# Performance work log

Measured on AMD Instinct MI355X. Metric: run time of the kernel, lower is better.

The kernel has to match this reference:

```python
import jax, jax.numpy as jnp
import numpy as np

NUM_HEADS = 4
NUM_GROUPS = 8
EPS = 1e-5


def group_norm(x, gamma, beta):
    B, C, H, W = x.shape
    xg = x.reshape(B, NUM_GROUPS, C // NUM_GROUPS, H, W)
    mean = xg.mean(axis=(2, 3, 4), keepdims=True)
    var = xg.var(axis=(2, 3, 4), keepdims=True)
    xn = ((xg - mean) * jax.lax.rsqrt(var + EPS)).reshape(B, C, H, W)
    return xn * gamma[None, :, None, None] + beta[None, :, None, None]


def setup_inputs() -> dict:
    key = jax.random.key(0)
    k1, k2, k3 = jax.random.split(key, 3)
    B, C, H, W = 16, 512, 32, 32
    x = jax.random.normal(k1, (B, C, H, W), dtype=jnp.float32)
    gn_gamma = jnp.ones((C,), dtype=jnp.float32)
    gn_beta = jnp.zeros((C,), dtype=jnp.float32)
    w_qkv = jax.random.normal(k2, (3 * C, C), dtype=jnp.float32) * 0.02
    w_proj = jax.random.normal(k3, (C, C), dtype=jnp.float32) * 0.02
    b_proj = jnp.zeros((C,), dtype=jnp.float32)
    return {"x": x, "gn_gamma": gn_gamma, "gn_beta": gn_beta,
            "w_qkv": w_qkv, "w_proj": w_proj, "b_proj": b_proj}


def reference(x, gn_gamma, gn_beta, w_qkv, w_proj, b_proj):
    B, C, H, W = x.shape
    nh = NUM_HEADS
    hd = C // nh
    N = H * W

    x_norm = group_norm(x, gn_gamma, gn_beta)
    # 1x1 conv == channel matmul: (B,C,H,W) x (3C,C) -> (B,3C,H,W)
    qkv = jnp.einsum('bchw,dc->bdhw', x_norm, w_qkv)
    qkv = qkv.reshape(B, 3, nh, hd, N)
    q, k, v = qkv[:, 0], qkv[:, 1], qkv[:, 2]  # each (B, nh, hd, N)

    scale = hd ** (-0.5)
    attn = jnp.einsum('bhci,bhcj->bhij', q, k) * scale  # (B, nh, N, N)
    attn = jax.nn.softmax(attn, axis=-1)
    out = jnp.einsum('bhij,bhcj->bhci', attn, v)  # (B, nh, hd, N)
    out = out.reshape(B, C, H, W)

    proj = jnp.einsum('bchw,dc->bdhw', out, w_proj) + b_proj[None, :, None, None]
    return x + proj
```

## Files before the change

### kernel.cpp

```cpp
#include <hip/hip_runtime.h>
#include <stdint.h>

typedef unsigned short u16;
typedef unsigned int u32;
typedef __attribute__((ext_vector_type(8))) short short8;
typedef __attribute__((ext_vector_type(4))) float f32x4;
typedef __attribute__((ext_vector_type(16))) float f32x16;

#define BATCH 16
#define CCH   512
#define NPIX  1024
#define NGRP  8
#define CPG   64
#define NHEAD 4
#define HDIM  128
#define KVBLK 64

__device__ __forceinline__ u16 f2bf(float f) {
  union { float f; u32 u; } v; v.f = f;
  u32 u = v.u;
  u32 r = (u + 0x7FFFu + ((u >> 16) & 1u)) >> 16;
  return (u16)r;
}

__device__ __forceinline__ void gload16(const void* g, void* l) {
  typedef __attribute__((address_space(3))) u32 L;
  typedef __attribute__((address_space(1))) const u32 G;
  __builtin_amdgcn_global_load_lds((G*)(uintptr_t)g, (L*)(u32)(uintptr_t)l, 16, 0, 0);
}

#define CVTPK(dst, a, b) asm("v_cvt_pk_bf16_f32 %0, %1, %2" : "=v"(dst) : "v"(a), "v"(b))
#define PLSWAP(a, b) asm("v_permlane32_swap_b32 %0, %1" : "+v"(a), "+v"(b))

__device__ __forceinline__ short8 rd512(const char* base, int r, int ck, int hi) {
  int byte = ((r >> 2) * 512) +
             ((((r & 3) * 128) + ck * 32 + hi * 16) ^ (((r >> 2) & 15) << 4));
  return *reinterpret_cast<const short8*>(base + byte);
}

__global__ void gn_stats_k(const float* __restrict__ x, float* __restrict__ part) {
  int bg = blockIdx.x >> 3, sl = blockIdx.x & 7;
  const float* p = x + (size_t)bg * (CPG * NPIX) + sl * 8192;
  float s = 0.f, ss = 0.f;
  for (int i = threadIdx.x; i < 2048; i += 256) {
    float4 v = reinterpret_cast<const float4*>(p)[i];
    s  += v.x + v.y + v.z + v.w;
    ss += v.x*v.x + v.y*v.y + v.z*v.z + v.w*v.w;
  }
  for (int o = 32; o > 0; o >>= 1) { s += __shfl_down(s, o); ss += __shfl_down(ss, o); }
  __shared__ float sh[8];
  int wid = threadIdx.x >> 6;
  if ((threadIdx.x & 63) == 0) { sh[wid*2] = s; sh[wid*2+1] = ss; }
  __syncthreads();
  if (threadIdx.x == 0) {
    part[blockIdx.x*2]   = sh[0]+sh[2]+sh[4]+sh[6];
    part[blockIdx.x*2+1] = sh[1]+sh[3]+sh[5]+sh[7];
  }
}

__global__ __launch_bounds__(256) void gn_apply_t(const float* __restrict__ x,
                                                  const float* __restrict__ gamma,
                                                  const float* __restrict__ beta,
                                                  const float* __restrict__ part,
                                                  u16* __restrict__ xnT) {
  const int p0 = blockIdx.x * 64;
  const int c0 = blockIdx.y * 64;
  const int b  = blockIdx.z;
  __shared__ float lt[64][66];

  const int bg = b * NGRP + (c0 >> 6);
  float s = 0.f, ss = 0.f;
  #pragma unroll
  for (int k2 = 0; k2 < 8; ++k2) { s += part[(bg*8 + k2)*2]; ss += part[(bg*8 + k2)*2 + 1]; }
  const float invn = 1.f / (float)(CPG * NPIX);
  const float mean = s * invn;
  const float rstd = rsqrtf(ss * invn - mean * mean + 1e-5f);

  const int t = threadIdx.x;
  #pragma unroll
  for (int pass = 0; pass < 4; ++pass) {
    int c   = c0 + (t >> 4) + pass * 16;
    int pix = p0 + (t & 15) * 4;
    float ga = gamma[c] * rstd;
    float be = beta[c] - mean * ga;
    float4 v = *reinterpret_cast<const float4*>(&x[((size_t)(b*CCH + c)) * NPIX + pix]);
    int pl = (t & 15) * 4, cl = (t >> 4) + pass * 16;
    lt[pl+0][cl] = v.x*ga + be;
    lt[pl+1][cl] = v.y*ga + be;
    lt[pl+2][cl] = v.z*ga + be;
    lt[pl+3][cl] = v.w*ga + be;
  }
  __syncthreads();
  const int pl = t >> 2, cq = (t & 3) * 16;
  u32 wbuf[8];
  #pragma unroll
  for (int e = 0; e < 8; ++e) {
    u16 lo = f2bf(lt[pl][cq + e*2]);
    u16 hi = f2bf(lt[pl][cq + e*2 + 1]);
    wbuf[e] = (u32)lo | ((u32)hi << 16);
  }
  u32* dst = (u32*)&xnT[((size_t)(b*NPIX + p0 + pl)) * CCH + c0 + cq];
  #pragma unroll
  for (int e = 0; e < 8; ++e) dst[e] = wbuf[e];
}

__global__ void f2bf_all(const float* __restrict__ wqkv, const float* __restrict__ wproj,
                         u16* __restrict__ wq, u16* __restrict__ wp, float qs) {
  int i = blockIdx.x * 256 + threadIdx.x;
  float4 v; u16* dst; float sc = 1.f;
  if (i < 196608) {
    v = reinterpret_cast<const float4*>(wqkv)[i];
    if (i < 65536) sc = qs;
    dst = wq + (size_t)i * 4;
  } else {
    v = reinterpret_cast<const float4*>(wproj)[i - 196608];
    dst = wp + (size_t)(i - 196608) * 4;
  }
  u32 lo = (u32)f2bf(v.x*sc) | ((u32)f2bf(v.y*sc) << 16);
  u32 hi = (u32)f2bf(v.z*sc) | ((u32)f2bf(v.w*sc) << 16);
  *reinterpret_cast<uint2*>(dst) = make_uint2(lo, hi);
}

__global__ __launch_bounds__(256, 3) void gemm_qkv(const u16* __restrict__ xnT,
                                                   const u16* __restrict__ wq_bf,
                                                   u16* __restrict__ outQ,
                                                   u16* __restrict__ outK,
                                                   u16* __restrict__ outV) {
  __shared__ __align__(16) char smem[34816];

  const int id = blockIdx.x;
  const int wg = (id & 7) * 192 + (id >> 3);
  const bool mode0 = (wg < 1024);
  int rt, ct;
  if (mode0) { rt = wg >> 3; ct = wg & 7; }
  else       { int w1 = wg - 1024; rt = w1 & 3; ct = w1 >> 2; }

  const char* Ab = mode0 ? (const char*)xnT + (size_t)rt * 131072
                         : (const char*)wq_bf + (size_t)(8 + rt) * 131072;
  const char* Bb = mode0 ? (const char*)wq_bf + (size_t)ct * 131072
                         : (const char*)xnT + (size_t)ct * 131072;

  const int t = threadIdx.x;
  const int lane = t & 63, w = t >> 6;
  const int q = lane & 31, hi = lane >> 5;
  const int rh = (w >> 1) * 64, ch = (w & 1) * 64;

  int soff[4];
  #pragma unroll
  for (int i = 0; i < 4; ++i) {
    int p = w*4096 + i*1024 + lane*16;
    int lrow = p >> 9, off = p & 511;
    int loff = off ^ ((lrow & 15) << 4);
    soff[i] = (lrow*4 + (loff >> 7)) * 1024 + (loff & 127);
  }

  f32x16 a00 = {}, a01 = {}, a10 = {}, a11 = {};

  for (int kt = 0; kt < 8; ++kt) {
    __syncthreads();
    #pragma unroll
    for (int i = 0; i < 4; ++i) {
      gload16(Ab + kt*128 + soff[i], smem + w*4096 + i*1024);
      gload16(Bb + kt*128 + soff[i], smem + 16384 + w*4096 + i*1024);
    }
    __syncthreads();
    #pragma unroll
    for (int ck = 0; ck < 4; ++ck) {
      short8 af0 = rd512(smem,         rh + q,      ck, hi);
      short8 af1 = rd512(smem,         rh + 32 + q, ck, hi);
      short8 bf0 = rd512(smem + 16384, ch + q,      ck, hi);
      short8 bf1 = rd512(smem + 16384, ch + 32 + q, ck, hi);
      a00 = __builtin_amdgcn_mfma_f32_32x32x16_bf16(af0, bf0, a00, 0, 0, 0);
      a01 = __builtin_amdgcn_mfma_f32_32x32x16_bf16(af0, bf1, a01, 0, 0, 0);
      a10 = __builtin_amdgcn_mfma_f32_32x32x16_bf16(af1, bf0, a10, 0, 0, 0);
      a11 = __builtin_amdgcn_mfma_f32_32x32x16_bf16(af1, bf1, a11, 0, 0, 0);
    }
  }

  __syncthreads();
  u16* Dt = (u16*)smem;
  #pragma unroll
  for (int r = 0; r < 16; ++r) {
    int ar = (r & 3) + 8*(r >> 2) + 4*hi;
    Dt[(rh +      ar) * 136 + ch +      q] = f2bf(a00[r]);
    Dt[(rh +      ar) * 136 + ch + 32 + q] = f2bf(a01[r]);
    Dt[(rh + 32 + ar) * 136 + ch +      q] = f2bf(a10[r]);
    Dt[(rh + 32 + ar) * 136 + ch + 32 + q] = f2bf(a11[r]);
  }
  __syncthreads();

  const int rl = t >> 1, hoff = (t & 1) * 64;
  uint4 buf[8];
  const uint4* s4 = reinterpret_cast<const uint4*>(&Dt[rl*136 + hoff]);
  #pragma unroll
  for (int e = 0; e < 8; ++e) buf[e] = s4[e];

  u16* gdst;
  if (mode0) {
    const int tok0 = rt * 128;
    const int b = tok0 >> 10, pix0 = tok0 & 1023;
    const int h = ct & 3;
    u16* base = (ct >= 4) ? outK : outQ;
    gdst = base + ((size_t)((b*NHEAD + h)) * NPIX + pix0 + rl) * HDIM + hoff;
  } else {
    const int m0 = rt * 128, tok0 = ct * 128;
    const int b = tok0 >> 10, pix0 = tok0 & 1023;
    gdst = outV + ((size_t)(b*CCH + m0 + rl)) * NPIX + pix0 + hoff;
  }
  uint4* g4 = reinterpret_cast<uint4*>(gdst);
  #pragma unroll
  for (int e = 0; e < 8; ++e) g4[e] = buf[e];
}

__global__ __launch_bounds__(256, 3) void gemm_proj(const u16* __restrict__ wp_bf,
                                                    const u16* __restrict__ attnO,
                                                    const float* __restrict__ xres,
                                                    const float* __restrict__ bias,
                                                    float* __restrict__ outF) {
  __shared__ __align__(16) char smem[32768];

  const int id = blockIdx.x;
  const int wg = (id & 7) * 64 + (id >> 3);
  const int rt = wg & 3, ct = wg >> 2;

  const char* Ab = (const char*)wp_bf + (size_t)rt * 131072;
  const char* Bb = (const char*)attnO + (size_t)ct * 131072;

  const int t = threadIdx.x;
  const int lane = t & 63, w = t >> 6;
  const int q = lane & 31, hi = lane >> 5;
  const int rh = (w >> 1) * 64, ch = (w & 1) * 64;

  int soff[4];
  #pragma unroll
  for (int i = 0; i < 4; ++i) {
    int p = w*4096 + i*1024 + lane*16;
    int lrow = p >> 9, off = p & 511;
    int loff = off ^ ((lrow & 15) << 4);
    soff[i] = (lrow*4 + (loff >> 7)) * 1024 + (loff & 127);
  }

  f32x16 a00 = {}, a01 = {}, a10 = {}, a11 = {};

  for (int kt = 0; kt < 8; ++kt) {
    __syncthreads();
    #pragma unroll
    for (int i = 0; i < 4; ++i) {
      gload16(Ab + kt*128 + soff[i], smem + w*4096 + i*1024);
      gload16(Bb + kt*128 + soff[i], smem + 16384 + w*4096 + i*1024);
    }
    __syncthreads();
    #pragma unroll
    for (int ck = 0; ck < 4; ++ck) {
      short8 af0 = rd512(smem,         rh + q,      ck, hi);
      short8 af1 = rd512(smem,         rh + 32 + q, ck, hi);
      short8 bf0 = rd512(smem + 16384, ch + q,      ck, hi);
      short8 bf1 = rd512(smem + 16384, ch + 32 + q, ck, hi);
      a00 = __builtin_amdgcn_mfma_f32_32x32x16_bf16(af0, bf0, a00, 0, 0, 0);
      a01 = __builtin_amdgcn_mfma_f32_32x32x16_bf16(af0, bf1, a01, 0, 0, 0);
      a10 = __builtin_amdgcn_mfma_f32_32x32x16_bf16(af1, bf0, a10, 0, 0, 0);
      a11 = __builtin_amdgcn_mfma_f32_32x32x16_bf16(af1, bf1, a11, 0, 0, 0);
    }
  }

  const int m0 = rt * 128, tok0 = ct * 128;
  const int b = tok0 >> 10, pix0 = tok0 & 1023;
  #pragma unroll
  for (int r = 0; r < 16; ++r) {
    int ar = (r & 3) + 8*(r >> 2) + 4*hi;
    int m0r = m0 + rh + ar, m1r = m0 + rh + 32 + ar;
    size_t o00 = ((size_t)(b*CCH + m0r)) * NPIX + pix0 + ch + q;
    size_t o01 = o00 + 32;
    size_t o10 = ((size_t)(b*CCH + m1r)) * NPIX + pix0 + ch + q;
    size_t o11 = o10 + 32;
    outF[o00] = xres[o00] + a00[r] + bias[m0r];
    outF[o01] = xres[o01] + a01[r] + bias[m0r];
    outF[o10] = xres[o10] + a10[r] + bias[m1r];
    outF[o11] = xres[o11] + a11[r] + bias[m1r];
  }
}

__global__ __launch_bounds__(256, 2) void attn_k(const u16* __restrict__ Qt,
                                                 const u16* __restrict__ Kt,
                                                 const u16* __restrict__ Vb,
                                                 u16* __restrict__ attnO) {
  int id = blockIdx.x;
  int swz = (id & 7) * 64 + (id >> 3);
  const int qt = swz & 7;
  const int h  = (swz >> 3) & 3;
  const int b  = swz >> 5;
  const int bh = b * NHEAD + h;

  __shared__ __align__(16) char smem[65536];

  const int t = threadIdx.x;
  const int lane = t & 63, w = t >> 6;
  const int q = lane & 31, hi = lane >> 5;

  const u16*  Qb    = Qt + ((size_t)bh * NPIX + qt*128 + w*32 + q) * HDIM;
  const char* Kbase = (const char*)(Kt + (size_t)bh * NPIX * HDIM);
  const char* Vbase = (const char*)(Vb + ((size_t)b*CCH + h*HDIM) * NPIX);

  short8 qf[8];
  #pragma unroll
  for (int ck = 0; ck < 8; ++ck)
    qf[ck] = *reinterpret_cast<const short8*>(&Qb[ck*16 + hi*8]);

  int koff[4], voff[4];
  #pragma unroll
  for (int i = 0; i < 4; ++i) {
    int d = w*4096 + i*1024 + lane*16;
    int r = d >> 8, cb = d & 255;
    int col = cb ^ ((r & 15) << 4);
    koff[i] = r*256 + col;
    int half = col >> 7, kvb = col & 127;
    voff[i] = (2*r + half)*2048 + kvb;
  }

  const int ksw = (q & 15) << 4;
  const int vsw = (q >> 1) << 4;

  f32x16 of0 = {}, of1 = {}, of2 = {}, of3 = {};
  float l_run = 0.f;
  short8 pf0, pf1, pf2, pf3;

  #pragma unroll
  for (int i = 0; i < 4; ++i) {
    gload16(Kbase + koff[i],            smem +         w*4096 + i*1024);
    gload16(Vbase + voff[i],            smem + 32768 + w*4096 + i*1024);
    gload16(Kbase + (size_t)64*256 + koff[i], smem + 16384 + w*4096 + i*1024);
  }
  asm volatile("s_waitcnt vmcnt(0)" ::: "memory");
  __syncthreads();

  f32x16 s0 = {}, s1 = {};
  #pragma unroll
  for (int ck = 0; ck < 8; ++ck) {
    const short8 kf0 = *reinterpret_cast<const short8*>(smem + q*256      + ((ck*32 + hi*16) ^ ksw));
    const short8 kf1 = *reinterpret_cast<const short8*>(smem + (32+q)*256 + ((ck*32 + hi*16) ^ ksw));
    s0 = __builtin_amdgcn_mfma_f32_32x32x16_bf16(kf0, qf[ck], s0, 0, 0, 0);
    s1 = __builtin_amdgcn_mfma_f32_32x32x16_bf16(kf1, qf[ck], s1, 0, 0, 0);
  }
  {
    float psum = 0.f;
    u32 wg[8], xg[8];
    #pragma unroll
    for (int u = 0; u < 8; ++u) {
      float pa = exp2f(s0[2*u]);  float pb = exp2f(s0[2*u+1]);
      float pc = exp2f(s1[2*u]);  float pd = exp2f(s1[2*u+1]);
      psum += (pa + pb) + (pc + pd);
      CVTPK(wg[u], pa, pb);
      CVTPK(xg[u], pc, pd);
    }
    psum += __shfl_xor(psum, 32);
    l_run += psum;
    PLSWAP(wg[0], wg[2]); PLSWAP(wg[1], wg[3]);
    PLSWAP(wg[4], wg[6]); PLSWAP(wg[5], wg[7]);
    PLSWAP(xg[0], xg[2]); PLSWAP(xg[1], xg[3]);
    PLSWAP(xg[4], xg[6]); PLSWAP(xg[5], xg[7]);
    union { u32 u[4]; short8 s; } a0, a1, a2, a3;
    #pragma unroll
    for (int u = 0; u < 4; ++u) { a0.u[u]=wg[u]; a1.u[u]=wg[4+u]; a2.u[u]=xg[u]; a3.u[u]=xg[4+u]; }
    pf0 = a0.s; pf1 = a1.s; pf2 = a2.s; pf3 = a3.s;
  }

  for (int tt = 0; tt < 16; ++tt) {
    asm volatile("s_waitcnt vmcnt(0)" ::: "memory");
    __syncthreads();

    char* kcur = smem + (((tt+1) & 1) << 14);
    char* vcur = smem + 32768 + ((tt & 1) << 14);

    if (tt + 1 < 16) {
      char* vdst = smem + 32768 + (((tt+1) & 1) << 14);
      #pragma unroll
      for (int i = 0; i < 4; ++i)
        gload16(Vbase + (size_t)(tt+1)*128 + voff[i], vdst + w*4096 + i*1024);
    }
    if (tt + 2 < 16) {
      char* kdst = smem + ((tt & 1) << 14);
      #pragma unroll
      for (int i = 0; i < 4; ++i)
        gload16(Kbase + (size_t)(tt+2)*64*256 + koff[i], kdst + w*4096 + i*1024);
    }

    __builtin_amdgcn_s_setprio(1);
    if (tt + 1 < 16) {
      s0 = {}; s1 = {};
      #pragma unroll
      for (int ck = 0; ck < 8; ++ck) {
        const short8 kf0 = *reinterpret_cast<const short8*>(kcur + q*256      + ((ck*32 + hi*16) ^ ksw));
        const short8 kf1 = *reinterpret_cast<const short8*>(kcur + (32+q)*256 + ((ck*32 + hi*16) ^ ksw));
        s0 = __builtin_amdgcn_mfma_f32_32x32x16_bf16(kf0, qf[ck], s0, 0, 0, 0);
        s1 = __builtin_amdgcn_mfma_f32_32x32x16_bf16(kf1, qf[ck], s1, 0, 0, 0);
      }
    }
    #pragma unroll
    for (int cg = 0; cg < 4; ++cg) {
      const char* vrow = vcur + (cg*16 + (q >> 1))*256;
      const int hb = (q & 1) << 7;
      f32x16 o = (cg == 0) ? of0 : (cg == 1) ? of1 : (cg == 2) ? of2 : of3;
      o = __builtin_amdgcn_mfma_f32_32x32x16_bf16(*reinterpret_cast<const short8*>(vrow + ((hb +  0 + hi*16) ^ vsw)), pf0, o, 0, 0, 0);
      o = __builtin_amdgcn_mfma_f32_32x32x16_bf16(*reinterpret_cast<const short8*>(vrow + ((hb + 32 + hi*16) ^ vsw)), pf1, o, 0, 0, 0);
      o = __builtin_amdgcn_mfma_f32_32x32x16_bf16(*reinterpret_cast<const short8*>(vrow + ((hb + 64 + hi*16) ^ vsw)), pf2, o, 0, 0, 0);
      o = __builtin_amdgcn_mfma_f32_32x32x16_bf16(*reinterpret_cast<const short8*>(vrow + ((hb + 96 + hi*16) ^ vsw)), pf3, o, 0, 0, 0);
      if (cg == 0) of0 = o; else if (cg == 1) of1 = o; else if (cg == 2) of2 = o; else of3 = o;
    }
    __builtin_amdgcn_s_setprio(0);

    if (tt + 1 < 16) {
      float psum = 0.f;
      u32 wg[8], xg[8];
      #pragma unroll
      for (int u = 0; u < 8; ++u) {
        float pa = exp2f(s0[2*u]);  float pb = exp2f(s0[2*u+1]);
        float pc = exp2f(s1[2*u]);  float pd = exp2f(s1[2*u+1]);
        psum += (pa + pb) + (pc + pd);
        CVTPK(wg[u], pa, pb);
        CVTPK(xg[u], pc, pd);
      }
      psum += __shfl_xor(psum, 32);
      l_run += psum;
      PLSWAP(wg[0], wg[2]); PLSWAP(wg[1], wg[3]);
      PLSWAP(wg[4], wg[6]); PLSWAP(wg[5], wg[7]);
      PLSWAP(xg[0], xg[2]); PLSWAP(xg[1], xg[3]);
      PLSWAP(xg[4], xg[6]); PLSWAP(xg[5], xg[7]);
      union { u32 u[4]; short8 s; } a0, a1, a2, a3;
      #pragma unroll
      for (int u = 0; u < 4; ++u) { a0.u[u]=wg[u]; a1.u[u]=wg[4+u]; a2.u[u]=xg[u]; a3.u[u]=xg[4+u]; }
      pf0 = a0.s; pf1 = a1.s; pf2 = a2.s; pf3 = a3.s;
    }
  }

  float inv = 1.f / l_run;
  u16* orow = attnO + ((size_t)(b*NPIX + qt*128 + w*32 + q)) * CCH + h*HDIM;
  #pragma unroll
  for (int cg = 0; cg < 4; ++cg) {
    const f32x16& o = (cg == 0) ? of0 : (cg == 1) ? of1 : (cg == 2) ? of2 : of3;
    #pragma unroll
    for (int u = 0; u < 8; ++u) {
      int c = cg*32 + ((2*u) & 3) + 8*(u >> 1) + 4*hi;
      u32 pk = (u32)f2bf(o[2*u] * inv) | ((u32)f2bf(o[2*u+1] * inv) << 16);
      *reinterpret_cast<u32*>(&orow[c]) = pk;
    }
  }
}

extern "C" void kernel_launch(void* const* d_in, const int* in_sizes, int n_in,
                              void* d_out, int out_size, void* d_ws, size_t ws_size,
                              hipStream_t stream) {
  const float* x     = (const float*)d_in[0];
  const float* gamma = (const float*)d_in[1];
  const float* beta  = (const float*)d_in[2];
  const float* wqkv  = (const float*)d_in[3];
  const float* wproj = (const float*)d_in[4];
  const float* bproj = (const float*)d_in[5];
  float* out = (float*)d_out;

  char* ws = (char*)d_ws;
  float* part   = (float*)ws;
  u16*   xnT    = (u16*)(ws + 8192);
  u16*   wq_bf  = (u16*)(ws + 8192 + (16u<<20));
  u16*   wp_bf  = (u16*)((char*)wq_bf + 1572864);
  u16*   Qt     = (u16*)((char*)wp_bf + 524288);
  u16*   Kt     = (u16*)((char*)Qt + (16u<<20));
  u16*   Vb     = (u16*)((char*)Kt + (16u<<20));
  u16*   attnO  = (u16*)((char*)Vb + (16u<<20));

  const float qs = 0.08838834764831845f * 1.44269504088896f;

  gn_stats_k<<<dim3(1024), dim3(256), 0, stream>>>(x, part);
  gn_apply_t<<<dim3(16, 8, BATCH), dim3(256), 0, stream>>>(x, gamma, beta, part, xnT);
  f2bf_all<<<dim3(1024), dim3(256), 0, stream>>>(wqkv, wproj, wq_bf, wp_bf, qs);

  gemm_qkv<<<dim3(1536), dim3(256), 0, stream>>>(xnT, wq_bf, Qt, Kt, Vb);

  attn_k<<<dim3(512), dim3(256), 0, stream>>>(Qt, Kt, Vb, attnO);

  gemm_proj<<<dim3(512), dim3(256), 0, stream>>>(wp_bf, attnO, x, bproj, out);
}
```

Baseline: 124.7 us.

## Double-buffer LDS tiles in QKV and projection GEMMs with async prefetch

The QKV and projection GEMM kernels now keep two LDS tile buffers (64KB total) so the next K-slice is fetched by global_load_lds while MFMAs run on the current one. This replaces the load-then-sync pattern that stalled on each tile. MFMA sections get raised wave priority. Occupancy hints drop from 3 to 2 blocks per CU because of the larger LDS footprint. The attention kernel's softmax/pack code is factored into a helper, with the row sum split across four partial accumulators.

```diff
diff --git a/kernel.cpp b/kernel.cpp
--- a/kernel.cpp
+++ b/kernel.cpp
@@ -6,6 +6,7 @@
 typedef __attribute__((ext_vector_type(8))) short short8;
 typedef __attribute__((ext_vector_type(4))) float f32x4;
 typedef __attribute__((ext_vector_type(16))) float f32x16;
+typedef __attribute__((ext_vector_type(4))) u32 u32x4;
 
 #define BATCH 16
 #define CCH   512
@@ -36,6 +37,31 @@
   int byte = ((r >> 2) * 512) +
              ((((r & 3) * 128) + ck * 32 + hi * 16) ^ (((r >> 2) & 15) << 4));
   return *reinterpret_cast<const short8*>(base + byte);
+}
+
+__device__ __forceinline__ float softmax_pack(const f32x16& s0, const f32x16& s1, short8* pf) {
+  float ps[4] = {0.f, 0.f, 0.f, 0.f};
+  u32 pw[16];
+  #pragma unroll
+  for (int u = 0; u < 8; ++u) {
+    float pa = exp2f(s0[2*u]);  float pb = exp2f(s0[2*u+1]);
+    float pc = exp2f(s1[2*u]);  float pd = exp2f(s1[2*u+1]);
+    ps[u & 3] += (pa + pb) + (pc + pd);
+    CVTPK(pw[u],     pa, pb);
+    CVTPK(pw[8 + u], pc, pd);
+  }
+  PLSWAP(pw[0], pw[2]);  PLSWAP(pw[1], pw[3]);
+  PLSWAP(pw[4], pw[6]);  PLSWAP(pw[5], pw[7]);
+  PLSWAP(pw[8], pw[10]); PLSWAP(pw[9], pw[11]);
+  PLSWAP(pw[12], pw[14]); PLSWAP(pw[13], pw[15]);
+  #pragma unroll
+  for (int f = 0; f < 4; ++f) {
+    u32x4 t = {pw[f*4], pw[f*4+1], pw[f*4+2], pw[f*4+3]};
+    pf[f] = __builtin_bit_cast(short8, t);
+  }
+  float psum = (ps[0] + ps[1]) + (ps[2] + ps[3]);
+  psum += __shfl_xor(psum, 32);
+  return psum;
 }
 
 __global__ void gn_stats_k(const float* __restrict__ x, float* __restrict__ part) {
@@ -121,12 +147,12 @@
   *reinterpret_cast<uint2*>(dst) = make_uint2(lo, hi);
 }
 
-__global__ __launch_bounds__(256, 3) void gemm_qkv(const u16* __restrict__ xnT,
+__global__ __launch_bounds__(256, 2) void gemm_qkv(const u16* __restrict__ xnT,
                                                    const u16* __restrict__ wq_bf,
                                                    u16* __restrict__ outQ,
                                                    u16* __restrict__ outK,
                                                    u16* __restrict__ outV) {
-  __shared__ __align__(16) char smem[34816];
+  __shared__ __align__(16) char smem[65536];
 
   const int id = blockIdx.x;
   const int wg = (id & 7) * 192 + (id >> 3);
@@ -154,27 +180,39 @@
     soff[i] = (lrow*4 + (loff >> 7)) * 1024 + (loff & 127);
   }
 
-  f32x16 a00 = {}, a01 = {}, a10 = {}, a11 = {};
+  #pragma unroll
+  for (int i = 0; i < 4; ++i) {
+    gload16(Ab + soff[i], smem +         w*4096 + i*1024);
+    gload16(Bb + soff[i], smem + 16384 + w*4096 + i*1024);
+  }
+
+  f32x16 acc[2][2] = {};
 
   for (int kt = 0; kt < 8; ++kt) {
+    asm volatile("s_waitcnt vmcnt(0)" ::: "memory");
     __syncthreads();
-    #pragma unroll
-    for (int i = 0; i < 4; ++i) {
-      gload16(Ab + kt*128 + soff[i], smem + w*4096 + i*1024);
-      gload16(Bb + kt*128 + soff[i], smem + 16384 + w*4096 + i*1024);
-    }
-    __syncthreads();
+    const char* cur = smem + (kt & 1) * 32768;
+    if (kt + 1 < 8) {
+      char* nxt = smem + ((kt + 1) & 1) * 32768;
+      #pragma unroll
+      for (int i = 0; i < 4; ++i) {
+        gload16(Ab + (kt+1)*128 + soff[i], nxt +         w*4096 + i*1024);
+        gload16(Bb + (kt+1)*128 + soff[i], nxt + 16384 + w*4096 + i*1024);
+      }
+    }
+    __builtin_amdgcn_s_setprio(1);
     #pragma unroll
     for (int ck = 0; ck < 4; ++ck) {
-      short8 af0 = rd512(smem,         rh + q,      ck, hi);
-      short8 af1 = rd512(smem,         rh + 32 + q, ck, hi);
-      short8 bf0 = rd512(smem + 16384, ch + q,      ck, hi);
-      short8 bf1 = rd512(smem + 16384, ch + 32 + q, ck, hi);
-      a00 = __builtin_amdgcn_mfma_f32_32x32x16_bf16(af0, bf0, a00, 0, 0, 0);
-      a01 = __builtin_amdgcn_mfma_f32_32x32x16_bf16(af0, bf1, a01, 0, 0, 0);
-      a10 = __builtin_amdgcn_mfma_f32_32x32x16_bf16(af1, bf0, a10, 0, 0, 0);
-      a11 = __builtin_amdgcn_mfma_f32_32x32x16_bf16(af1, bf1, a11, 0, 0, 0);
-    }
+      short8 af0 = rd512(cur,         rh + q,      ck, hi);
+      short8 af1 = rd512(cur,         rh + 32 + q, ck, hi);
+      short8 bf0 = rd512(cur + 16384, ch + q,      ck, hi);
+      short8 bf1 = rd512(cur + 16384, ch + 32 + q, ck, hi);
+      acc[0][0] = __builtin_amdgcn_mfma_f32_32x32x16_bf16(af0, bf0, acc[0][0], 0, 0, 0);
+      acc[0][1] = __builtin_amdgcn_mfma_f32_32x32x16_bf16(af0, bf1, acc[0][1], 0, 0, 0);
+      acc[1][0] = __builtin_amdgcn_mfma_f32_32x32x16_bf16(af1, bf0, acc[1][0], 0, 0, 0);
+      acc[1][1] = __builtin_amdgcn_mfma_f32_32x32x16_bf16(af1, bf1, acc[1][1], 0, 0, 0);
+    }
+    __builtin_amdgcn_s_setprio(0);
   }
 
   __syncthreads();
@@ -182,10 +220,10 @@
   #pragma unroll
   for (int r = 0; r < 16; ++r) {
     int ar = (r & 3) + 8*(r >> 2) + 4*hi;
-    Dt[(rh +      ar) * 136 + ch +      q] = f2bf(a00[r]);
-    Dt[(rh +      ar) * 136 + ch + 32 + q] = f2bf(a01[r]);
-    Dt[(rh + 32 + ar) * 136 + ch +      q] = f2bf(a10[r]);
-    Dt[(rh + 32 + ar) * 136 + ch + 32 + q] = f2bf(a11[r]);
+    Dt[(rh +      ar) * 136 + ch +      q] = f2bf(acc[0][0][r]);
+    Dt[(rh +      ar) * 136 + ch + 32 + q] = f2bf(acc[0][1][r]);
+    Dt[(rh + 32 + ar) * 136 + ch +      q] = f2bf(acc[1][0][r]);
+    Dt[(rh + 32 + ar) * 136 + ch + 32 + q] = f2bf(acc[1][1][r]);
   }
   __syncthreads();
 
@@ -212,12 +250,12 @@
   for (int e = 0; e < 8; ++e) g4[e] = buf[e];
 }
 
-__global__ __launch_bounds__(256, 3) void gemm_proj(const u16* __restrict__ wp_bf,
+__global__ __launch_bounds__(256, 2) void gemm_proj(const u16* __restrict__ wp_bf,
                                                     const u16* __restrict__ attnO,
                                                     const float* __restrict__ xres,
                                                     const float* __restrict__ bias,
                                                     float* __restrict__ outF) {
-  __shared__ __align__(16) char smem[32768];
+  __shared__ __align__(16) char smem[65536];
 
   const int id = blockIdx.x;
   const int wg = (id & 7) * 64 + (id >> 3);
@@ -240,27 +278,39 @@
     soff[i] = (lrow*4 + (loff >> 7)) * 1024 + (loff & 127);
   }
 
-  f32x16 a00 = {}, a01 = {}, a10 = {}, a11 = {};
+  #pragma unroll
+  for (int i = 0; i < 4; ++i) {
+    gload16(Ab + soff[i], smem +         w*4096 + i*1024);
+    gload16(Bb + soff[i], smem + 16384 + w*4096 + i*1024);
+  }
+
+  f32x16 acc[2][2] = {};
 
   for (int kt = 0; kt < 8; ++kt) {
+    asm volatile("s_waitcnt vmcnt(0)" ::: "memory");
     __syncthreads();
-    #pragma unroll
-    for (int i = 0; i < 4; ++i) {
-      gload16(Ab + kt*128 + soff[i], smem + w*4096 + i*1024);
-      gload16(Bb + kt*128 + soff[i], smem + 16384 + w*4096 + i*1024);
-    }
-    __syncthreads();
+    const char* cur = smem + (kt & 1) * 32768;
+    if (kt + 1 < 8) {
+      char* nxt = smem + ((kt + 1) & 1) * 32768;
+      #pragma unroll
+      for (int i = 0; i < 4; ++i) {
+        gload16(Ab + (kt+1)*128 + soff[i], nxt +         w*4096 + i*1024);
+        gload16(Bb + (kt+1)*128 + soff[i], nxt + 16384 + w*4096 + i*1024);
+      }
+    }
+    __builtin_amdgcn_s_setprio(1);
     #pragma unroll
     for (int ck = 0; ck < 4; ++ck) {
-      short8 af0 = rd512(smem,         rh + q,      ck, hi);
-      short8 af1 = rd512(smem,         rh + 32 + q, ck, hi);
-      short8 bf0 = rd512(smem + 16384, ch + q,      ck, hi);
-      short8 bf1 = rd512(smem + 16384, ch + 32 + q, ck, hi);
-      a00 = __builtin_amdgcn_mfma_f32_32x32x16_bf16(af0, bf0, a00, 0, 0, 0);
-      a01 = __builtin_amdgcn_mfma_f32_32x32x16_bf16(af0, bf1, a01, 0, 0, 0);
-      a10 = __builtin_amdgcn_mfma_f32_32x32x16_bf16(af1, bf0, a10, 0, 0, 0);
-      a11 = __builtin_amdgcn_mfma_f32_32x32x16_bf16(af1, bf1, a11, 0, 0, 0);
-    }
+      short8 af0 = rd512(cur,         rh + q,      ck, hi);
+      short8 af1 = rd512(cur,         rh + 32 + q, ck, hi);
+      short8 bf0 = rd512(cur + 16384, ch + q,      ck, hi);
+      short8 bf1 = rd512(cur + 16384, ch + 32 + q, ck, hi);
+      acc[0][0] = __builtin_amdgcn_mfma_f32_32x32x16_bf16(af0, bf0, acc[0][0], 0, 0, 0);
+      acc[0][1] = __builtin_amdgcn_mfma_f32_32x32x16_bf16(af0, bf1, acc[0][1], 0, 0, 0);
+      acc[1][0] = __builtin_amdgcn_mfma_f32_32x32x16_bf16(af1, bf0, acc[1][0], 0, 0, 0);
+      acc[1][1] = __builtin_amdgcn_mfma_f32_32x32x16_bf16(af1, bf1, acc[1][1], 0, 0, 0);
+    }
+    __builtin_amdgcn_s_setprio(0);
   }
 
   const int m0 = rt * 128, tok0 = ct * 128;
@@ -273,10 +323,10 @@
     size_t o01 = o00 + 32;
     size_t o10 = ((size_t)(b*CCH + m1r)) * NPIX + pix0 + ch + q;
     size_t o11 = o10 + 32;
-    outF[o00] = xres[o00] + a00[r] + bias[m0r];
-    outF[o01] = xres[o01] + a01[r] + bias[m0r];
-    outF[o10] = xres[o10] + a10[r] + bias[m1r];
-    outF[o11] = xres[o11] + a11[r] + bias[m1r];
+    outF[o00] = xres[o00] + acc[0][0][r] + bias[m0r];
+    outF[o01] = xres[o01] + acc[0][1][r] + bias[m0r];
+    outF[o10] = xres[o10] + acc[1][0][r] + bias[m1r];
+    outF[o11] = xres[o11] + acc[1][1][r] + bias[m1r];
   }
 }
 
@@ -320,56 +370,37 @@
   const int ksw = (q & 15) << 4;
   const int vsw = (q >> 1) << 4;
 
-  f32x16 of0 = {}, of1 = {}, of2 = {}, of3 = {};
+  f32x16 of[4] = {};
   float l_run = 0.f;
-  short8 pf0, pf1, pf2, pf3;
-
-  #pragma unroll
-  for (int i = 0; i < 4; ++i) {
-    gload16(Kbase + koff[i],            smem +         w*4096 + i*1024);
-    gload16(Vbase + voff[i],            smem + 32768 + w*4096 + i*1024);
+  short8 pf[4];
+
+  #pragma unroll
+  for (int i = 0; i < 4; ++i) {
+    gload16(Kbase + koff[i],                  smem +         w*4096 + i*1024);
+    gload16(Vbase + voff[i],                  smem + 32768 + w*4096 + i*1024);
     gload16(Kbase + (size_t)64*256 + koff[i], smem + 16384 + w*4096 + i*1024);
   }
   asm volatile("s_waitcnt vmcnt(0)" ::: "memory");
   __syncthreads();
 
-  f32x16 s0 = {}, s1 = {};
-  #pragma unroll
-  for (int ck = 0; ck < 8; ++ck) {
-    const short8 kf0 = *reinterpret_cast<const short8*>(smem + q*256      + ((ck*32 + hi*16) ^ ksw));
-    const short8 kf1 = *reinterpret_cast<const short8*>(smem + (32+q)*256 + ((ck*32 + hi*16) ^ ksw));
-    s0 = __builtin_amdgcn_mfma_f32_32x32x16_bf16(kf0, qf[ck], s0, 0, 0, 0);
-    s1 = __builtin_amdgcn_mfma_f32_32x32x16_bf16(kf1, qf[ck], s1, 0, 0, 0);
-  }
   {
-    float psum = 0.f;
-    u32 wg[8], xg[8];
+    f32x16 sn[2] = {};
     #pragma unroll
-    for (int u = 0; u < 8; ++u) {
-      float pa = exp2f(s0[2*u]);  float pb = exp2f(s0[2*u+1]);
-      float pc = exp2f(s1[2*u]);  float pd = exp2f(s1[2*u+1]);
-      psum += (pa + pb) + (pc + pd);
-      CVTPK(wg[u], pa, pb);
-      CVTPK(xg[u], pc, pd);
-    }
-    psum += __shfl_xor(psum, 32);
-    l_run += psum;
-    PLSWAP(wg[0], wg[2]); PLSWAP(wg[1], wg[3]);
-    PLSWAP(wg[4], wg[6]); PLSWAP(wg[5], wg[7]);
-    PLSWAP(xg[0], xg[2]); PLSWAP(xg[1], xg[3]);
-    PLSWAP(xg[4], xg[6]); PLSWAP(xg[5], xg[7]);
-    union { u32 u[4]; short8 s; } a0, a1, a2, a3;
-    #pragma unroll
-    for (int u = 0; u < 4; ++u) { a0.u[u]=wg[u]; a1.u[u]=wg[4+u]; a2.u[u]=xg[u]; a3.u[u]=xg[4+u]; }
-    pf0 = a0.s; pf1 = a1.s; pf2 = a2.s; pf3 = a3.s;
+    for (int ck = 0; ck < 8; ++ck) {
+      const short8 kf0 = *reinterpret_cast<const short8*>(smem + q*256      + ((ck*32 + hi*16) ^ ksw));
+      const short8 kf1 = *reinterpret_cast<const short8*>(smem + (32+q)*256 + ((ck*32 + hi*16) ^ ksw));
+      sn[0] = __builtin_amdgcn_mfma_f32_32x32x16_bf16(kf0, qf[ck], sn[0], 0, 0, 0);
+      sn[1] = __builtin_amdgcn_mfma_f32_32x32x16_bf16(kf1, qf[ck], sn[1], 0, 0, 0);
+    }
+    l_run += softmax_pack(sn[0], sn[1], pf);
   }
 
   for (int tt = 0; tt < 16; ++tt) {
     asm volatile("s_waitcnt vmcnt(0)" ::: "memory");
     __syncthreads();
 
-    char* kcur = smem + (((tt+1) & 1) << 14);
-    char* vcur = smem + 32768 + ((tt & 1) << 14);
+    const char* kcur = smem + (((tt+1) & 1) << 14);
+    const char* vcur = smem + 32768 + ((tt & 1) << 14);
 
     if (tt + 1 < 16) {
       char* vdst = smem + 32768 + (((tt+1) & 1) << 14);
@@ -384,63 +415,41 @@
         gload16(Kbase + (size_t)(tt+2)*64*256 + koff[i], kdst + w*4096 + i*1024);
     }
 
+    f32x16 sn[2] = {};
     __builtin_amdgcn_s_setprio(1);
     if (tt + 1 < 16) {
-      s0 = {}; s1 = {};
       #pragma unroll
       for (int ck = 0; ck < 8; ++ck) {
         const short8 kf0 = *reinterpret_cast<const short8*>(kcur + q*256      + ((ck*32 + hi*16) ^ ksw));
         const short8 kf1 = *reinterpret_cast<const short8*>(kcur + (32+q)*256 + ((ck*32 + hi*16) ^ ksw));
-        s0 = __builtin_amdgcn_mfma_f32_32x32x16_bf16(kf0, qf[ck], s0, 0, 0, 0);
-        s1 = __builtin_amdgcn_mfma_f32_32x32x16_bf16(kf1, qf[ck], s1, 0, 0, 0);
+        sn[0] = __builtin_amdgcn_mfma_f32_32x32x16_bf16(kf0, qf[ck], sn[0], 0, 0, 0);
+        sn[1] = __builtin_amdgcn_mfma_f32_32x32x16_bf16(kf1, qf[ck], sn[1], 0, 0, 0);
       }
     }
     #pragma unroll
     for (int cg = 0; cg < 4; ++cg) {
       const char* vrow = vcur + (cg*16 + (q >> 1))*256;
       const int hb = (q & 1) << 7;
-      f32x16 o = (cg == 0) ? of0 : (cg == 1) ? of1 : (cg == 2) ? of2 : of3;
-      o = __builtin_amdgcn_mfma_f32_32x32x16_bf16(*reinterpret_cast<const short8*>(vrow + ((hb +  0 + hi*16) ^ vsw)), pf0, o, 0, 0, 0);
-      o = __builtin_amdgcn_mfma_f32_32x32x16_bf16(*reinterpret_cast<const short8*>(vrow + ((hb + 32 + hi*16) ^ vsw)), pf1, o, 0, 0, 0);
-      o = __builtin_amdgcn_mfma_f32_32x32x16_bf16(*reinterpret_cast<const short8*>(vrow + ((hb + 64 + hi*16) ^ vsw)), pf2, o, 0, 0, 0);
-      o = __builtin_amdgcn_mfma_f32_32x32x16_bf16(*reinterpret_cast<const short8*>(vrow + ((hb + 96 + hi*16) ^ vsw)), pf3, o, 0, 0, 0);
-      if (cg == 0) of0 = o; else if (cg == 1) of1 = o; else if (cg == 2) of2 = o; else of3 = o;
+      #pragma unroll
+      for (int kc = 0; kc < 4; ++kc)
+        of[cg] = __builtin_amdgcn_mfma_f32_32x32x16_bf16(
+            *reinterpret_cast<const short8*>(vrow + ((hb + kc*32 + hi*16) ^ vsw)),
+            pf[kc], of[cg], 0, 0, 0);
     }
     __builtin_amdgcn_s_setprio(0);
 
-    if (tt + 1 < 16) {
-      float psum = 0.f;
-      u32 wg[8], xg[8];
-      #pragma unroll
-      for (int u = 0; u < 8; ++u) {
-        float pa = exp2f(s0[2*u]);  float pb = exp2f(s0[2*u+1]);
-        float pc = exp2f(s1[2*u]);  float pd = exp2f(s1[2*u+1]);
-        psum += (pa + pb) + (pc + pd);
-        CVTPK(wg[u], pa, pb);
-        CVTPK(xg[u], pc, pd);
-      }
-      psum += __shfl_xor(psum, 32);
-      l_run += psum;
-      PLSWAP(wg[0], wg[2]); PLSWAP(wg[1], wg[3]);
-      PLSWAP(wg[4], wg[6]); PLSWAP(wg[5], wg[7]);
-      PLSWAP(xg[0], xg[2]); PLSWAP(xg[1], xg[3]);
-      PLSWAP(xg[4], xg[6]); PLSWAP(xg[5], xg[7]);
-      union { u32 u[4]; short8 s; } a0, a1, a2, a3;
-      #pragma unroll
-      for (int u = 0; u < 4; ++u) { a0.u[u]=wg[u]; a1.u[u]=wg[4+u]; a2.u[u]=xg[u]; a3.u[u]=xg[4+u]; }
-      pf0 = a0.s; pf1 = a1.s; pf2 = a2.s; pf3 = a3.s;
-    }
+    if (tt + 1 < 16)
+      l_run += softmax_pack(sn[0], sn[1], pf);
   }
 
   float inv = 1.f / l_run;
   u16* orow = attnO + ((size_t)(b*NPIX + qt*128 + w*32 + q)) * CCH + h*HDIM;
   #pragma unroll
   for (int cg = 0; cg < 4; ++cg) {
-    const f32x16& o = (cg == 0) ? of0 : (cg == 1) ? of1 : (cg == 2) ? of2 : of3;
     #pragma unroll
     for (int u = 0; u < 8; ++u) {
       int c = cg*32 + ((2*u) & 3) + 8*(u >> 1) + 4*hi;
-      u32 pk = (u32)f2bf(o[2*u] * inv) | ((u32)f2bf(o[2*u+1] * inv) << 16);
+      u32 pk = (u32)f2bf(of[cg][2*u] * inv) | ((u32)f2bf(of[cg][2*u+1] * inv) << 16);
       *reinterpret_cast<u32*>(&orow[c]) = pk;
     }
   }
```

After: 123.3 us. Within noise of the previous version (-1.1%).
